# Kernel tuning notes

Measured on AMD Instinct MI355X. Metric: run time of the kernel, lower is better.

The kernel has to match this reference:

```python
import jax, jax.numpy as jnp
import numpy as np

B, N, C, H = 2, 2048, 1024, 16
D = C // H  # head dim
SCALE = D ** -0.5


def setup_inputs() -> dict:
    key = jax.random.key(0)
    k1, k2, k3 = jax.random.split(key, 3)
    x = jax.random.normal(k1, (B, N, C), dtype=jnp.float32)
    w_qkv = jax.random.normal(k2, (C, 3 * C), dtype=jnp.float32) * (C ** -0.5)
    w_proj = jax.random.normal(k3, (C, C), dtype=jnp.float32) * (C ** -0.5)
    b_proj = jnp.zeros((C,), dtype=jnp.float32)
    return {"x": x, "w_qkv": w_qkv, "w_proj": w_proj, "b_proj": b_proj}


def reference(x, w_qkv, w_proj, b_proj):
    # qkv projection: [B,N,3C] -> [3,B,H,N,D]
    qkv = (x @ w_qkv).reshape(B, N, 3, H, D).transpose(2, 0, 3, 1, 4)
    q, k, v = qkv[0], qkv[1], qkv[2]
    # attention scores [B,H,N,N]
    attn = jnp.einsum("bhnd,bhmd->bhnm", q, k) * SCALE
    attn = jax.nn.softmax(attn, axis=-1)
    # weighted values -> [B,N,C]
    out = jnp.einsum("bhnm,bhmd->bhnd", attn, v)
    out = out.transpose(0, 2, 1, 3).reshape(B, N, C)
    return out @ w_proj + b_proj
```

## Files before the change

kernel.cpp:

```cpp
#include <hip/hip_runtime.h>
#include <hip/hip_bf16.h>

#define BDIM 2
#define NSEQ 2048
#define CDIM 1024
#define HNUM 16
#define DDIM 64
#define QSCALE 0.18033688f

typedef __attribute__((ext_vector_type(4))) float f4;
typedef __attribute__((ext_vector_type(8))) short s8;

__device__ __forceinline__ unsigned short f2bf_hi(float f) {
  unsigned int u = __float_as_uint(f);
  u += 0x7fffu + ((u >> 16) & 1u);
  return (unsigned short)(u >> 16);
}
__device__ __forceinline__ float bf2f(unsigned short s) {
  return __uint_as_float(((unsigned int)s) << 16);
}
__device__ __forceinline__ void split2(float f, short& h, short& l) {
  unsigned short hs = f2bf_hi(f);
  h = (short)hs;
  l = (short)f2bf_hi(f - bf2f(hs));
}
__device__ __forceinline__ unsigned int pack_bf16x2(float lo, float hi) {
  __hip_bfloat162 b2 = __float22bfloat162_rn(float2{lo, hi});
  union { __hip_bfloat162 b; unsigned int u; } c;
  c.b = b2;
  return c.u;
}
__device__ __forceinline__ float exp2_raw(float x) {
  float r;
  asm("v_exp_f32 %0, %1" : "=v"(r) : "v"(x));
  return r;
}
__device__ __forceinline__ void gll16(const void* g, void* l) {
  __builtin_amdgcn_global_load_lds(
      (const __attribute__((address_space(1))) unsigned int*)g,
      (__attribute__((address_space(3))) unsigned int*)l, 16, 0, 0);
}

__global__ __launch_bounds__(256)
void split_xh(const float* __restrict__ X, short* __restrict__ Xh) {
  size_t i = ((size_t)blockIdx.x * 256 + threadIdx.x) * 8;
  f4 a = *(const f4*)(X + i), b = *(const f4*)(X + i + 4);
  s8 h;
  #pragma unroll
  for (int j = 0; j < 4; ++j) h[j] = (short)f2bf_hi(a[j]);
  #pragma unroll
  for (int j = 0; j < 4; ++j) h[4 + j] = (short)f2bf_hi(b[j]);
  *(s8*)(Xh + i) = h;
}

__global__ __launch_bounds__(256)
void tsplit(const float* __restrict__ W, short* __restrict__ Th, short* __restrict__ Tl, int N) {
  __shared__ float T[64][65];
  const int t = threadIdx.x;
  const int c0 = blockIdx.x * 64, k0 = blockIdx.y * 64;
  const int r = t >> 2, c16 = (t & 3) * 16;
  const float* src = W + (size_t)(k0 + r) * N + c0 + c16;
  #pragma unroll
  for (int q = 0; q < 4; ++q) {
    f4 v = *(const f4*)(src + q * 4);
    #pragma unroll
    for (int j = 0; j < 4; ++j) T[c16 + q * 4 + j][r] = v[j];
  }
  __syncthreads();
  const int rr = t >> 2, k16 = (t & 3) * 16;
  s8 h0, h1, l0, l1;
  #pragma unroll
  for (int j = 0; j < 8; ++j) { short hh, ll; split2(T[rr][k16 + j], hh, ll); h0[j] = hh; l0[j] = ll; }
  #pragma unroll
  for (int j = 0; j < 8; ++j) { short hh, ll; split2(T[rr][k16 + 8 + j], hh, ll); h1[j] = hh; l1[j] = ll; }
  size_t o = (size_t)(c0 + rr) * 1024 + k0 + k16;
  *(s8*)(Th + o) = h0;
  *(s8*)(Th + o + 8) = h1;
  if (Tl != nullptr) {
    *(s8*)(Tl + o) = l0;
    *(s8*)(Tl + o + 8) = l1;
  }
}

__global__ __launch_bounds__(256)
void transpose_v(const short* __restrict__ Vh, short* __restrict__ Vt) {
  __shared__ short T[64][72];
  const int t = threadIdx.x;
  const int n0 = blockIdx.x * 64, bh = blockIdx.y;
  const int r = t >> 2, dc = (t & 3) * 16;
  const short* src = Vh + ((size_t)bh * 2048 + n0 + r) * 64 + dc;
  s8 a = *(const s8*)src, b = *(const s8*)(src + 8);
  #pragma unroll
  for (int j = 0; j < 8; ++j) { T[dc + j][r] = a[j]; T[dc + 8 + j][r] = b[j]; }
  __syncthreads();
  const int d = t >> 2, n16 = (t & 3) * 16;
  s8 x, y;
  #pragma unroll
  for (int j = 0; j < 8; ++j) { x[j] = T[d][n16 + j]; y[j] = T[d][n16 + 8 + j]; }
  short* dst = Vt + ((size_t)bh * 64 + d) * 2048 + n0 + n16;
  *(s8*)dst = x;
  *(s8*)(dst + 8) = y;
}

__global__ __launch_bounds__(256, 3)
void gemm_qkv(const short* __restrict__ Ah_g, const short* __restrict__ Bth,
              short* __restrict__ Qh, short* __restrict__ Kh, short* __restrict__ Vh)
{
  __shared__ __align__(16) short lds[2][2][128 * 32];
  const int t = threadIdx.x, w = t >> 6, lane = t & 63;
  const int fr = lane & 15, g = lane >> 4;
  const int wr = (w >> 1) * 64, wc = (w & 1) * 64;
  const int m0 = blockIdx.y * 128, c0 = blockIdx.x * 128;

  f4 acc[4][4];
  #pragma unroll
  for (int i = 0; i < 4; ++i)
    #pragma unroll
    for (int j = 0; j < 4; ++j)
      #pragma unroll
      for (int r = 0; r < 4; ++r) acc[i][j][r] = 0.f;

  auto stage = [&](int buf, int kt) {
    const int k0 = kt * 32;
    #pragma unroll
    for (int p = 0; p < 4; ++p) {
      const int plane = p >> 1;
      const int cid = (p & 1) * 256 + t;
      const int r = cid >> 2, c = cid & 3;
      const short* gsrc = (plane == 0)
          ? Ah_g + (size_t)(m0 + r) * 1024 + k0 + c * 8
          : Bth + (size_t)(c0 + r) * 1024 + k0 + c * 8;
      gll16(gsrc, &lds[buf][plane][(p & 1) * 2048 + w * 512]);
    }
  };

  auto compute = [&](int buf) {
    const short* A_h = lds[buf][0];
    const short* B_h = lds[buf][1];
    s8 ah[4], bh[4];
    #pragma unroll
    for (int i = 0; i < 4; ++i) ah[i] = *(const s8*)&A_h[(wr + i * 16 + fr) * 32 + g * 8];
    #pragma unroll
    for (int j = 0; j < 4; ++j) bh[j] = *(const s8*)&B_h[(wc + j * 16 + fr) * 32 + g * 8];
    #pragma unroll
    for (int i = 0; i < 4; ++i)
      #pragma unroll
      for (int j = 0; j < 4; ++j)
        acc[i][j] = __builtin_amdgcn_mfma_f32_16x16x32_bf16(ah[i], bh[j], acc[i][j], 0, 0, 0);
  };

  stage(0, 0);
  __syncthreads();
  int cur = 0;
  for (int kt = 0; kt < 32; ++kt) {
    if (kt + 1 < 32) stage(cur ^ 1, kt + 1);
    compute(cur);
    __syncthreads();
    cur ^= 1;
  }

  const int ts = c0 >> 10;
  const int rbase = g * 4;
  #pragma unroll
  for (int i = 0; i < 4; ++i)
    #pragma unroll
    for (int j = 0; j < 4; ++j)
      #pragma unroll
      for (int rr = 0; rr < 4; ++rr) {
        int grow = m0 + wr + i * 16 + rbase + rr;
        int gcol = c0 + wc + j * 16 + fr;
        int b = grow >> 11, n = grow & 2047;
        int rem = gcol & 1023, hh = rem >> 6, d = rem & 63;
        size_t o = (((size_t)(b * 16 + hh)) * 2048 + n) * 64 + d;
        float v = acc[i][j][rr];
        if (ts == 0)      Qh[o] = (short)f2bf_hi(v * QSCALE);
        else if (ts == 1) Kh[o] = (short)f2bf_hi(v);
        else              Vh[o] = (short)f2bf_hi(v);
      }
}

__global__ __launch_bounds__(512, 2)
void attn(const short* __restrict__ Qh, const short* __restrict__ Kh,
          const short* __restrict__ Vt,
          short* __restrict__ AOh)
{
  __shared__ __align__(16) short kb[2][64 * 64], vb[2][64 * 64];
  __shared__ __align__(16) short pb[8][16][88];
  const int t = threadIdx.x, w = t >> 6, lane = t & 63;
  const int fr = lane & 15, g = lane >> 4;
  const int bid = blockIdx.x;
  const int swz = (bid & 7) * 64 + (bid >> 3);
  const int bh = swz >> 4, qb = swz & 15, q0 = qb * 128;
  const size_t base = (size_t)bh * 2048 * 64;

  s8 qf[2];
  {
    const int qrow = q0 + w * 16 + fr;
    #pragma unroll
    for (int ks = 0; ks < 2; ++ks)
      qf[ks] = *(const s8*)(Qh + base + (size_t)qrow * 64 + ks * 32 + g * 8);
  }

  float l_run = 0.f;
  f4 oacc[4];
  #pragma unroll
  for (int dj = 0; dj < 4; ++dj)
    #pragma unroll
    for (int r = 0; r < 4; ++r) oacc[dj][r] = 0.f;

  auto stage = [&](int buf, int kt) {
    const int kv0 = kt * 64;
    const int r = t >> 3, csw = t & 7, cl = csw ^ (r & 7);
    gll16(Kh + base + (size_t)(kv0 + r) * 64 + cl * 8, &kb[buf][t * 8]);
    gll16(Vt + base + (size_t)r * 2048 + kv0 + cl * 8, &vb[buf][t * 8]);
  };

  auto body = [&](const short* kbuf, const short* vbuf) {
    f4 st[4];
    #pragma unroll
    for (int j = 0; j < 4; ++j)
      #pragma unroll
      for (int r = 0; r < 4; ++r) st[j][r] = 0.f;
    __builtin_amdgcn_s_setprio(1);
    #pragma unroll
    for (int j = 0; j < 4; ++j) {
      const int R = j * 16 + fr;
      #pragma unroll
      for (int ks = 0; ks < 2; ++ks) {
        const int co = ((ks * 4 + g) ^ (R & 7)) * 8;
        s8 khf = *(const s8*)&kbuf[R * 64 + co];
        st[j] = __builtin_amdgcn_mfma_f32_16x16x32_bf16(khf, qf[ks], st[j], 0, 0, 0);
      }
    }
    __builtin_amdgcn_s_setprio(0);

    float rs = 0.f;
    #pragma unroll
    for (int j = 0; j < 4; ++j)
      #pragma unroll
      for (int r = 0; r < 4; ++r) {
        float p = exp2_raw(st[j][r]);
        st[j][r] = p;
        rs += p;
      }
    rs += __shfl_xor(rs, 16);
    rs += __shfl_xor(rs, 32);
    l_run += rs;

    #pragma unroll
    for (int j = 0; j < 4; ++j)
      #pragma unroll
      for (int rp = 0; rp < 2; ++rp)
        *(unsigned int*)&pb[w][fr][j * 16 + g * 4 + 2 * rp] =
            pack_bf16x2(st[j][2 * rp], st[j][2 * rp + 1]);

    __builtin_amdgcn_s_setprio(1);
    #pragma unroll
    for (int ks = 0; ks < 2; ++ks) {
      s8 paf = *(const s8*)&pb[w][fr][ks * 32 + g * 8];
      #pragma unroll
      for (int dj = 0; dj < 4; ++dj) {
        const int R = dj * 16 + fr;
        const int co = ((ks * 4 + g) ^ (R & 7)) * 8;
        s8 vbf = *(const s8*)&vbuf[R * 64 + co];
        oacc[dj] = __builtin_amdgcn_mfma_f32_16x16x32_bf16(paf, vbf, oacc[dj], 0, 0, 0);
      }
    }
    __builtin_amdgcn_s_setprio(0);
  };

  stage(0, 0);
  for (int kt = 0; kt < 32; kt += 2) {
    __syncthreads();
    stage(1, kt + 1);
    body(kb[0], vb[0]);
    __syncthreads();
    if (kt + 2 < 32) stage(0, kt + 2);
    body(kb[1], vb[1]);
  }

  const int b = bh >> 4, h = bh & 15;
  float linv[4];
  #pragma unroll
  for (int r = 0; r < 4; ++r) linv[r] = 1.f / __shfl(l_run, g * 4 + r);
  #pragma unroll
  for (int dj = 0; dj < 4; ++dj)
    #pragma unroll
    for (int rr = 0; rr < 4; ++rr) {
      int n = q0 + w * 16 + g * 4 + rr;
      int col = h * 64 + dj * 16 + fr;
      size_t o = ((size_t)b * 2048 + n) * 1024 + col;
      AOh[o] = (short)f2bf_hi(oacc[dj][rr] * linv[rr]);
    }
}

__global__ __launch_bounds__(256, 2)
void gemm_proj(const short* __restrict__ Ah_g, const short* __restrict__ Bth,
               const float* __restrict__ bias, float* __restrict__ OUT)
{
  __shared__ __align__(16) short la[2][4096], lb[2][2048];
  const int t = threadIdx.x, w = t >> 6, lane = t & 63;
  const int fr = lane & 15, g = lane >> 4;
  const int wr = (w >> 1) * 64, wc = (w & 1) * 32;
  const int m0 = blockIdx.y * 128, c0 = blockIdx.x * 64;

  f4 acc[4][2];
  #pragma unroll
  for (int i = 0; i < 4; ++i)
    #pragma unroll
    for (int j = 0; j < 2; ++j)
      #pragma unroll
      for (int r = 0; r < 4; ++r) acc[i][j][r] = 0.f;

  auto stage = [&](int buf, int kt) {
    const int k0 = kt * 32;
    #pragma unroll
    for (int p = 0; p < 2; ++p) {
      const int cid = p * 256 + t;
      const int r = cid >> 2, c = cid & 3;
      gll16(Ah_g + (size_t)(m0 + r) * 1024 + k0 + c * 8, la[buf] + cid * 8);
    }
    {
      const int r = t >> 2, c = t & 3;
      gll16(Bth + (size_t)(c0 + r) * 1024 + k0 + c * 8, lb[buf] + t * 8);
    }
  };

  auto compute = [&](int buf) {
    s8 ah[4], bhf[2];
    #pragma unroll
    for (int i = 0; i < 4; ++i) ah[i] = *(const s8*)&la[buf][(wr + i * 16 + fr) * 32 + g * 8];
    #pragma unroll
    for (int j = 0; j < 2; ++j) bhf[j] = *(const s8*)&lb[buf][(wc + j * 16 + fr) * 32 + g * 8];
    #pragma unroll
    for (int i = 0; i < 4; ++i)
      #pragma unroll
      for (int j = 0; j < 2; ++j)
        acc[i][j] = __builtin_amdgcn_mfma_f32_16x16x32_bf16(ah[i], bhf[j], acc[i][j], 0, 0, 0);
  };

  stage(0, 0);
  __syncthreads();
  int cur = 0;
  for (int kt = 0; kt < 32; ++kt) {
    if (kt + 1 < 32) stage(cur ^ 1, kt + 1);
    compute(cur);
    __syncthreads();
    cur ^= 1;
  }

  const int rbase = g * 4;
  #pragma unroll
  for (int i = 0; i < 4; ++i)
    #pragma unroll
    for (int j = 0; j < 2; ++j)
      #pragma unroll
      for (int rr = 0; rr < 4; ++rr) {
        int grow = m0 + wr + i * 16 + rbase + rr;
        int gcol = c0 + wc + j * 16 + fr;
        OUT[(size_t)grow * 1024 + gcol] = acc[i][j][rr] + bias[gcol];
      }
}

extern "C" void kernel_launch(void* const* d_in, const int* in_sizes, int n_in,
                              void* d_out, int out_size, void* d_ws, size_t ws_size,
                              hipStream_t stream) {
  const float* x      = (const float*)d_in[0];
  const float* w_qkv  = (const float*)d_in[1];
  const float* w_proj = (const float*)d_in[2];
  const float* b_proj = (const float*)d_in[3];
  short* ws = (short*)d_ws;

  const size_t SW = (size_t)3072 * 1024;
  const size_t SP = (size_t)1024 * 1024;
  const size_t SX = (size_t)4096 * 1024;
  short* Wqh = ws;
  short* Wph = Wqh + SW;
  short* Xh  = Wph + SP;
  short* Qh  = Xh + SX;
  short* Kh  = Qh + SX;
  short* Vh  = Kh + SX;
  short* Vt  = Xh;
  short* AOh = Vh;

  split_xh<<<2048, 256, 0, stream>>>(x, Xh);
  tsplit<<<dim3(48, 16), 256, 0, stream>>>(w_qkv, Wqh, nullptr, 3072);
  tsplit<<<dim3(16, 16), 256, 0, stream>>>(w_proj, Wph, nullptr, 1024);
  gemm_qkv<<<dim3(24, 32), 256, 0, stream>>>(Xh, Wqh, Qh, Kh, Vh);
  transpose_v<<<dim3(32, 32), 256, 0, stream>>>(Vh, Vt);
  attn<<<512, 512, 0, stream>>>(Qh, Kh, Vt, AOh);
  gemm_proj<<<dim3(16, 32), 256, 0, stream>>>(AOh, Wph, b_proj, (float*)d_out);
}
```

Before: 133.3 us.

## Merge prep kernels and write V transposed directly from QKV GEMM epilogue

Folds the three conversion kernels (x to bf16, w_qkv and w_proj transpose-to-bf16) into one launch that picks its role from the block index. It also removes the separate transpose_v kernel by having the QKV GEMM epilogue write V straight into [b,h,d,n] layout with 4-wide short stores. The aim is to cut kernel launch overhead and one full read-write pass over V. The cost is that the V epilogue stores are strided across the d dimension, so each 8-byte store lands in a different row.

```diff
diff --git a/kernel.cpp b/kernel.cpp
--- a/kernel.cpp
+++ b/kernel.cpp
@@ -16,14 +16,6 @@
   u += 0x7fffu + ((u >> 16) & 1u);
   return (unsigned short)(u >> 16);
 }
-__device__ __forceinline__ float bf2f(unsigned short s) {
-  return __uint_as_float(((unsigned int)s) << 16);
-}
-__device__ __forceinline__ void split2(float f, short& h, short& l) {
-  unsigned short hs = f2bf_hi(f);
-  h = (short)hs;
-  l = (short)f2bf_hi(f - bf2f(hs));
-}
 __device__ __forceinline__ unsigned int pack_bf16x2(float lo, float hi) {
   __hip_bfloat162 b2 = __float22bfloat162_rn(float2{lo, hi});
   union { __hip_bfloat162 b; unsigned int u; } c;
@@ -42,69 +34,65 @@
 }
 
 __global__ __launch_bounds__(256)
-void split_xh(const float* __restrict__ X, short* __restrict__ Xh) {
-  size_t i = ((size_t)blockIdx.x * 256 + threadIdx.x) * 8;
-  f4 a = *(const f4*)(X + i), b = *(const f4*)(X + i + 4);
-  s8 h;
-  #pragma unroll
-  for (int j = 0; j < 4; ++j) h[j] = (short)f2bf_hi(a[j]);
-  #pragma unroll
-  for (int j = 0; j < 4; ++j) h[4 + j] = (short)f2bf_hi(b[j]);
-  *(s8*)(Xh + i) = h;
-}
-
-__global__ __launch_bounds__(256)
-void tsplit(const float* __restrict__ W, short* __restrict__ Th, short* __restrict__ Tl, int N) {
+void prep(const float* __restrict__ X, const float* __restrict__ Wq,
+          const float* __restrict__ Wp,
+          short* __restrict__ Xh, short* __restrict__ Wqh, short* __restrict__ Wph)
+{
   __shared__ float T[64][65];
+  const int bx = blockIdx.x;
   const int t = threadIdx.x;
-  const int c0 = blockIdx.x * 64, k0 = blockIdx.y * 64;
-  const int r = t >> 2, c16 = (t & 3) * 16;
-  const float* src = W + (size_t)(k0 + r) * N + c0 + c16;
-  #pragma unroll
-  for (int q = 0; q < 4; ++q) {
-    f4 v = *(const f4*)(src + q * 4);
-    #pragma unroll
-    for (int j = 0; j < 4; ++j) T[c16 + q * 4 + j][r] = v[j];
+
+  if (bx < 2048) {
+    size_t i = ((size_t)bx * 256 + t) * 8;
+    f4 a = *(const f4*)(X + i), b = *(const f4*)(X + i + 4);
+    s8 h;
+    #pragma unroll
+    for (int j = 0; j < 4; ++j) h[j] = (short)f2bf_hi(a[j]);
+    #pragma unroll
+    for (int j = 0; j < 4; ++j) h[4 + j] = (short)f2bf_hi(b[j]);
+    *(s8*)(Xh + i) = h;
+    return;
+  }
+
+  const float* W;
+  short* Th;
+  int N, c0, k0;
+  if (bx < 2816) {
+    int b2 = bx - 2048;
+    W = Wq; Th = Wqh; N = 3072;
+    c0 = (b2 % 48) * 64; k0 = (b2 / 48) * 64;
+  } else {
+    int b2 = bx - 2816;
+    W = Wp; Th = Wph; N = 1024;
+    c0 = (b2 & 15) * 64; k0 = (b2 >> 4) * 64;
+  }
+  {
+    const int r = t >> 2, c16 = (t & 3) * 16;
+    const float* src = W + (size_t)(k0 + r) * N + c0 + c16;
+    #pragma unroll
+    for (int q = 0; q < 4; ++q) {
+      f4 v = *(const f4*)(src + q * 4);
+      #pragma unroll
+      for (int j = 0; j < 4; ++j) T[c16 + q * 4 + j][r] = v[j];
+    }
   }
   __syncthreads();
-  const int rr = t >> 2, k16 = (t & 3) * 16;
-  s8 h0, h1, l0, l1;
-  #pragma unroll
-  for (int j = 0; j < 8; ++j) { short hh, ll; split2(T[rr][k16 + j], hh, ll); h0[j] = hh; l0[j] = ll; }
-  #pragma unroll
-  for (int j = 0; j < 8; ++j) { short hh, ll; split2(T[rr][k16 + 8 + j], hh, ll); h1[j] = hh; l1[j] = ll; }
-  size_t o = (size_t)(c0 + rr) * 1024 + k0 + k16;
-  *(s8*)(Th + o) = h0;
-  *(s8*)(Th + o + 8) = h1;
-  if (Tl != nullptr) {
-    *(s8*)(Tl + o) = l0;
-    *(s8*)(Tl + o + 8) = l1;
-  }
-}
-
-__global__ __launch_bounds__(256)
-void transpose_v(const short* __restrict__ Vh, short* __restrict__ Vt) {
-  __shared__ short T[64][72];
-  const int t = threadIdx.x;
-  const int n0 = blockIdx.x * 64, bh = blockIdx.y;
-  const int r = t >> 2, dc = (t & 3) * 16;
-  const short* src = Vh + ((size_t)bh * 2048 + n0 + r) * 64 + dc;
-  s8 a = *(const s8*)src, b = *(const s8*)(src + 8);
-  #pragma unroll
-  for (int j = 0; j < 8; ++j) { T[dc + j][r] = a[j]; T[dc + 8 + j][r] = b[j]; }
-  __syncthreads();
-  const int d = t >> 2, n16 = (t & 3) * 16;
-  s8 x, y;
-  #pragma unroll
-  for (int j = 0; j < 8; ++j) { x[j] = T[d][n16 + j]; y[j] = T[d][n16 + 8 + j]; }
-  short* dst = Vt + ((size_t)bh * 64 + d) * 2048 + n0 + n16;
-  *(s8*)dst = x;
-  *(s8*)(dst + 8) = y;
+  {
+    const int rr = t >> 2, k16 = (t & 3) * 16;
+    s8 h0, h1;
+    #pragma unroll
+    for (int j = 0; j < 8; ++j) h0[j] = (short)f2bf_hi(T[rr][k16 + j]);
+    #pragma unroll
+    for (int j = 0; j < 8; ++j) h1[j] = (short)f2bf_hi(T[rr][k16 + 8 + j]);
+    size_t o = (size_t)(c0 + rr) * 1024 + k0 + k16;
+    *(s8*)(Th + o) = h0;
+    *(s8*)(Th + o + 8) = h1;
+  }
 }
 
 __global__ __launch_bounds__(256, 3)
 void gemm_qkv(const short* __restrict__ Ah_g, const short* __restrict__ Bth,
-              short* __restrict__ Qh, short* __restrict__ Kh, short* __restrict__ Vh)
+              short* __restrict__ Qh, short* __restrict__ Kh, short* __restrict__ Vt)
 {
   __shared__ __align__(16) short lds[2][2][128 * 32];
   const int t = threadIdx.x, w = t >> 6, lane = t & 63;
@@ -161,22 +149,39 @@
 
   const int ts = c0 >> 10;
   const int rbase = g * 4;
-  #pragma unroll
-  for (int i = 0; i < 4; ++i)
-    #pragma unroll
-    for (int j = 0; j < 4; ++j)
-      #pragma unroll
-      for (int rr = 0; rr < 4; ++rr) {
-        int grow = m0 + wr + i * 16 + rbase + rr;
+  if (ts == 2) {
+    #pragma unroll
+    for (int i = 0; i < 4; ++i)
+      #pragma unroll
+      for (int j = 0; j < 4; ++j) {
+        int grow = m0 + wr + i * 16 + rbase;
         int gcol = c0 + wc + j * 16 + fr;
         int b = grow >> 11, n = grow & 2047;
         int rem = gcol & 1023, hh = rem >> 6, d = rem & 63;
-        size_t o = (((size_t)(b * 16 + hh)) * 2048 + n) * 64 + d;
-        float v = acc[i][j][rr];
-        if (ts == 0)      Qh[o] = (short)f2bf_hi(v * QSCALE);
-        else if (ts == 1) Kh[o] = (short)f2bf_hi(v);
-        else              Vh[o] = (short)f2bf_hi(v);
-      }
+        short4 pv;
+        pv.x = (short)f2bf_hi(acc[i][j][0]);
+        pv.y = (short)f2bf_hi(acc[i][j][1]);
+        pv.z = (short)f2bf_hi(acc[i][j][2]);
+        pv.w = (short)f2bf_hi(acc[i][j][3]);
+        *(short4*)(Vt + (((size_t)(b * 16 + hh)) * 64 + d) * 2048 + n) = pv;
+      }
+  } else {
+    #pragma unroll
+    for (int i = 0; i < 4; ++i)
+      #pragma unroll
+      for (int j = 0; j < 4; ++j)
+        #pragma unroll
+        for (int rr = 0; rr < 4; ++rr) {
+          int grow = m0 + wr + i * 16 + rbase + rr;
+          int gcol = c0 + wc + j * 16 + fr;
+          int b = grow >> 11, n = grow & 2047;
+          int rem = gcol & 1023, hh = rem >> 6, d = rem & 63;
+          size_t o = (((size_t)(b * 16 + hh)) * 2048 + n) * 64 + d;
+          float v = acc[i][j][rr];
+          if (ts == 0) Qh[o] = (short)f2bf_hi(v * QSCALE);
+          else         Kh[o] = (short)f2bf_hi(v);
+        }
+  }
 }
 
 __global__ __launch_bounds__(512, 2)
@@ -379,15 +384,11 @@
   short* Xh  = Wph + SP;
   short* Qh  = Xh + SX;
   short* Kh  = Qh + SX;
-  short* Vh  = Kh + SX;
-  short* Vt  = Xh;
-  short* AOh = Vh;
-
-  split_xh<<<2048, 256, 0, stream>>>(x, Xh);
-  tsplit<<<dim3(48, 16), 256, 0, stream>>>(w_qkv, Wqh, nullptr, 3072);
-  tsplit<<<dim3(16, 16), 256, 0, stream>>>(w_proj, Wph, nullptr, 1024);
-  gemm_qkv<<<dim3(24, 32), 256, 0, stream>>>(Xh, Wqh, Qh, Kh, Vh);
-  transpose_v<<<dim3(32, 32), 256, 0, stream>>>(Vh, Vt);
+  short* Vt  = Kh + SX;
+  short* AOh = Xh;
+
+  prep<<<3072, 256, 0, stream>>>(x, w_qkv, w_proj, Xh, Wqh, Wph);
+  gemm_qkv<<<dim3(24, 32), 256, 0, stream>>>(Xh, Wqh, Qh, Kh, Vt);
   attn<<<512, 512, 0, stream>>>(Qh, Kh, Vt, AOh);
   gemm_proj<<<dim3(16, 32), 256, 0, stream>>>(AOh, Wph, b_proj, (float*)d_out);
 }
```

After: 119.6 us. 1.11x faster.
